# Performance work log

Measured on AMD Instinct MI355X. Metric: run time of the kernel, lower is better.

## Reference

```python
import jax, jax.numpy as jnp
import numpy as np

N = 50000   # nodes
E = 800000  # edges
H = 4       # num_heads
D = 32      # out_dim
IN = 256    # in_dim


def setup_inputs() -> dict:
    key = jax.random.key(0)
    k0, k1, k2, k3, k4, k5 = jax.random.split(key, 6)
    h = jax.random.normal(k0, (N, IN), dtype=jnp.float32)
    # fl weight (torch Linear stores [out, in]), xavier-ish scale
    Wl = jax.random.normal(k1, (H * D, IN), dtype=jnp.float32) * (1.0 / np.sqrt(IN))
    # fc / fq are initialized to small constants in torch; use small random here
    fc = jax.random.normal(k2, (IN, H * D), dtype=jnp.float32) * 0.02
    fq = jax.random.normal(k3, (IN, H * D), dtype=jnp.float32) * 0.02
    src = jax.random.randint(k4, (E,), 0, N)
    dst = jax.random.randint(k5, (E,), 0, N)
    return {"h": h, "Wl": Wl, "fc": fc, "fq": fq, "src": src, "dst": dst}


def reference(h, Wl, fc, fq, src, dst):
    n = h.shape[0]
    ft = (h @ Wl.T).reshape(n, H, D)      # [N,H,D]
    ft_c = (h @ fc).reshape(n, H, D)      # [N,H,D]
    ft_q = (h @ fq).reshape(n, H, D)      # [N,H,D]

    # edge attention: c = ft_c[dst], q = ft_q[src] - c, a = ELU(sum(q*c))
    c = ft_c[dst]                         # [E,H,D]
    a = jax.nn.elu(jnp.sum((ft_q[src] - c) * c, axis=-1))  # [E,H]

    # segmented (per-destination) softmax over incoming edges, per head
    m = jax.ops.segment_max(a, dst, num_segments=n)        # [N,H]
    ex = jnp.exp(a - m[dst])
    s = jax.ops.segment_sum(ex, dst, num_segments=n)       # [N,H]
    attn = ex / s[dst]                                     # [E,H]

    # global top-k (smallest l_s) threshold + mass redistribution, per head
    l_s = int(0.713 * attn.shape[0])
    srt = jnp.sort(attn, axis=0)                           # ascending per head
    thd = srt[l_s - 1]                                     # [H] l_s-th smallest
    topk_sum = jnp.sum(srt[:l_s], axis=0)                  # [H]
    a2 = jnp.where(attn - thd < 0, jnp.zeros((), attn.dtype), attn)
    ratio = (jnp.sum(a2, axis=0) + topk_sum) / jnp.sum(a2, axis=0)  # [H]
    a3 = a2 * ratio                                        # [E,H]

    # weighted scatter-sum of source features to destinations
    out = jax.ops.segment_sum(ft[src] * a3[:, :, None], dst, num_segments=n)  # [N,H,D]

    # concat=True: cat(flattened heads, mean over heads of ft)
    return jnp.concatenate([out.reshape(n, -1), ft.mean(axis=1)], axis=1)  # [N, H*D + D]
```

## Files before the change

kernel.cpp:

```cpp
#include <hip/hip_runtime.h>
#include <hip/hip_bf16.h>
#include <math.h>

#define N_NODES 50000
#define N_EDGES 800000
#define NH 4
#define DH 32
#define IN_DIM 256
#define OUTC 160
#define LS 570400
#define RANK0 (LS - 1)
#define DEG_CAP 160

typedef unsigned long long u64;
#define SC_FX 1099511627776.0

__global__ void k_deg(const int* __restrict__ dst, unsigned* __restrict__ A){
  int e = blockIdx.x * 256 + threadIdx.x;
  if (e < N_EDGES) atomicAdd(&A[dst[e]], 1u);
}

__global__ __launch_bounds__(1024) void k_scan(unsigned* __restrict__ A){
  __shared__ unsigned ps[1024];
  int t = threadIdx.x;
  const int CH = (N_NODES + 1023) / 1024;
  int base = t * CH;
  unsigned s = 0;
  for (int i = 0; i < CH; i++){ int n = base + i; if (n < N_NODES) s += A[n]; }
  ps[t] = s;
  __syncthreads();
  for (int off = 1; off < 1024; off <<= 1){
    unsigned v = (t >= off) ? ps[t - off] : 0;
    __syncthreads();
    ps[t] += v;
    __syncthreads();
  }
  unsigned ex = (t == 0) ? 0 : ps[t - 1];
  for (int i = 0; i < CH; i++){
    int n = base + i;
    if (n < N_NODES){ unsigned dv = A[n]; A[n] = ex; ex += dv; }
  }
}

__global__ void k_fill(const int* __restrict__ dst, unsigned* __restrict__ A,
                       unsigned* __restrict__ eidx){
  int e = blockIdx.x * 256 + threadIdx.x;
  if (e < N_EDGES) eidx[atomicAdd(&A[dst[e]], 1u)] = (unsigned)e;
}

__global__ void k_init(u64* __restrict__ sel4, unsigned* __restrict__ krem,
                       unsigned* __restrict__ cnt, unsigned* __restrict__ done,
                       unsigned* __restrict__ ccnt, u64* __restrict__ gsums){
  int t = threadIdx.x;
  if (t < 4){ sel4[t] = 0; krem[t] = RANK0; cnt[t] = 0; ccnt[t] = 0; }
  if (t < 8) gsums[t] = 0;
  if (t == 0) done[0] = 0;
}

#define BM 128
#define BK 16
__global__ __launch_bounds__(256) void k_gemm32(const float* __restrict__ A,
                                                const float* __restrict__ Wl,
                                                float* __restrict__ C){
  __shared__ float As[BK][BM + 4];
  __shared__ float Bs[BK][128 + 4];
  int tid = threadIdx.x;
  int m0 = blockIdx.x * BM;
  int ty = tid / 16, tx = tid % 16;
  float acc[8][8];
  #pragma unroll
  for (int i = 0; i < 8; i++)
    #pragma unroll
    for (int j = 0; j < 8; j++) acc[i][j] = 0.f;

  for (int k0 = 0; k0 < IN_DIM; k0 += BK){
    #pragma unroll
    for (int i = 0; i < 2; i++){
      int s = tid * 2 + i;
      int row = s >> 2, c4 = s & 3;
      int r = m0 + row;
      float4 v = make_float4(0.f, 0.f, 0.f, 0.f);
      if (r < N_NODES) v = *(const float4*)&A[(size_t)r * IN_DIM + k0 + c4 * 4];
      As[c4 * 4 + 0][row] = v.x; As[c4 * 4 + 1][row] = v.y;
      As[c4 * 4 + 2][row] = v.z; As[c4 * 4 + 3][row] = v.w;
    }
    #pragma unroll
    for (int i = 0; i < 2; i++){
      int s = tid * 2 + i;
      int j = s >> 2, c4 = s & 3;
      float4 v = *(const float4*)&Wl[(size_t)j * IN_DIM + k0 + c4 * 4];
      Bs[c4 * 4 + 0][j] = v.x; Bs[c4 * 4 + 1][j] = v.y;
      Bs[c4 * 4 + 2][j] = v.z; Bs[c4 * 4 + 3][j] = v.w;
    }
    __syncthreads();
    #pragma unroll
    for (int kk = 0; kk < BK; kk++){
      float4 a0 = *(const float4*)&As[kk][ty * 4];
      float4 a1 = *(const float4*)&As[kk][64 + ty * 4];
      float4 b0 = *(const float4*)&Bs[kk][tx * 4];
      float4 b1 = *(const float4*)&Bs[kk][64 + tx * 4];
      float av[8] = {a0.x, a0.y, a0.z, a0.w, a1.x, a1.y, a1.z, a1.w};
      float bv[8] = {b0.x, b0.y, b0.z, b0.w, b1.x, b1.y, b1.z, b1.w};
      #pragma unroll
      for (int i = 0; i < 8; i++)
        #pragma unroll
        for (int j = 0; j < 8; j++)
          acc[i][j] = fmaf(av[i], bv[j], acc[i][j]);
    }
    __syncthreads();
  }
  #pragma unroll
  for (int i = 0; i < 8; i++){
    int r = m0 + ((i < 4) ? (ty * 4 + i) : (64 + ty * 4 + (i - 4)));
    if (r >= N_NODES) continue;
    *(float4*)&C[(size_t)r * 128 + tx * 4]      = make_float4(acc[i][0], acc[i][1], acc[i][2], acc[i][3]);
    *(float4*)&C[(size_t)r * 128 + 64 + tx * 4] = make_float4(acc[i][4], acc[i][5], acc[i][6], acc[i][7]);
  }
}

__global__ __launch_bounds__(256) void k_gemm64(const float* __restrict__ A,
                                                const float* __restrict__ fc,
                                                const float* __restrict__ fq,
                                                double* __restrict__ c64,
                                                double* __restrict__ q64){
  __shared__ double As[16][66];
  __shared__ double Bs[16][66];
  int tid = threadIdx.x;
  int m0 = blockIdx.x * 64;
  int n0 = blockIdx.y * 64;
  const float* Bsrc = (n0 < 128) ? fc : fq;
  int j0 = (n0 < 128) ? n0 : n0 - 128;
  double* Cp = (n0 < 128) ? c64 : q64;
  int ty = tid / 16, tx = tid % 16;
  double acc[4][4];
  #pragma unroll
  for (int i = 0; i < 4; i++)
    #pragma unroll
    for (int j = 0; j < 4; j++) acc[i][j] = 0.0;

  for (int k0 = 0; k0 < IN_DIM; k0 += 16){
    {
      int row = tid >> 2, c4 = tid & 3;
      int r = m0 + row;
      float4 v = make_float4(0.f, 0.f, 0.f, 0.f);
      if (r < N_NODES) v = *(const float4*)&A[(size_t)r * IN_DIM + k0 + c4 * 4];
      As[c4 * 4 + 0][row] = (double)v.x; As[c4 * 4 + 1][row] = (double)v.y;
      As[c4 * 4 + 2][row] = (double)v.z; As[c4 * 4 + 3][row] = (double)v.w;
    }
    {
      int kr = tid >> 4, c4 = tid & 15;
      float4 v = *(const float4*)&Bsrc[(size_t)(k0 + kr) * 128 + j0 + c4 * 4];
      Bs[kr][c4 * 4 + 0] = (double)v.x; Bs[kr][c4 * 4 + 1] = (double)v.y;
      Bs[kr][c4 * 4 + 2] = (double)v.z; Bs[kr][c4 * 4 + 3] = (double)v.w;
    }
    __syncthreads();
    #pragma unroll
    for (int kk = 0; kk < 16; kk++){
      double a[4], b[4];
      #pragma unroll
      for (int i = 0; i < 4; i++) a[i] = As[kk][ty * 4 + i];
      #pragma unroll
      for (int j = 0; j < 4; j++) b[j] = Bs[kk][tx * 4 + j];
      #pragma unroll
      for (int i = 0; i < 4; i++)
        #pragma unroll
        for (int j = 0; j < 4; j++)
          acc[i][j] = fma(a[i], b[j], acc[i][j]);
    }
    __syncthreads();
  }
  #pragma unroll
  for (int i = 0; i < 4; i++){
    int r = m0 + ty * 4 + i;
    if (r >= N_NODES) continue;
    double* p = &Cp[(size_t)r * 128 + j0 + tx * 4];
    *(double2*)p       = make_double2(acc[i][0], acc[i][1]);
    *(double2*)(p + 2) = make_double2(acc[i][2], acc[i][3]);
  }
}

__global__ __launch_bounds__(256) void k_softedge(const double* __restrict__ c64,
    const double* __restrict__ q64, const int* __restrict__ src,
    const unsigned* __restrict__ A, const unsigned* __restrict__ eidx,
    double* __restrict__ abuf){
  __shared__ double lds_a[4][DEG_CAP * 4];
  int d = blockIdx.x * 4 + (threadIdx.x >> 6);
  int t = threadIdx.x & 63;
  int wv = threadIdx.x >> 6;
  if (d >= N_NODES) return;
  unsigned k0 = d ? A[d - 1] : 0u, k1 = A[d];
  if (k0 == k1) return;
  double2 c = *(const double2*)&c64[(size_t)d * 128 + t * 2];
  double m = -1.0e300;
  int sn = src[eidx[k0]];
  double2 qn = *(const double2*)&q64[(size_t)sn * 128 + t * 2];
  for (unsigned k = k0; k < k1; k++){
    double2 q = qn;
    if (k + 1 < k1){
      int s2 = src[eidx[k + 1]];
      qn = *(const double2*)&q64[(size_t)s2 * 128 + t * 2];
    }
    double val = (q.x - c.x) * c.x + (q.y - c.y) * c.y;
    val += __shfl_xor(val, 1);
    val += __shfl_xor(val, 2);
    val += __shfl_xor(val, 4);
    val += __shfl_xor(val, 8);
    double a = (val > 0.0) ? val : expm1(val);
    m = fmax(m, a);
    if ((t & 15) == 0) lds_a[wv][(k - k0) * 4 + (t >> 4)] = a;
  }
  double mm = __shfl(m, (t & 3) * 16);
  unsigned nj = (k1 - k0) * 4;
  long long sfx = 0;
  for (unsigned jj = t; jj < nj; jj += 64){
    double ex = exp(lds_a[wv][jj] - mm);
    lds_a[wv][jj] = ex;
    sfx += llrint(ex * SC_FX);
  }
  #pragma unroll
  for (int msk = 4; msk < 64; msk <<= 1) sfx += __shfl_xor(sfx, msk);
  double sd = (double)sfx * (1.0 / SC_FX);
  for (unsigned jj = t; jj < nj; jj += 64)
    abuf[(size_t)k0 * 4 + jj] = lds_a[wv][jj] / sd;
}

__global__ __launch_bounds__(256) void k_hp(const double* __restrict__ attn,
    u64* __restrict__ sel4, unsigned* __restrict__ krem, unsigned* __restrict__ cnt,
    unsigned* __restrict__ hist, unsigned* __restrict__ done, u64 maskHi, int shift){
  __shared__ unsigned lh[1024];
  __shared__ unsigned ticket;
  for (int j = threadIdx.x; j < 1024; j += 256) lh[j] = 0;
  __syncthreads();
  int i0 = blockIdx.x * 256 + threadIdx.x;
  int hh = i0 & 3;
  u64 sel = sel4[hh] & maskHi;
  const int total = N_EDGES * 4;
  for (int i = i0; i < total; i += gridDim.x * 256){
    u64 u = (u64)__double_as_longlong(attn[i]);
    if ((u & maskHi) == sel)
      atomicAdd(&lh[hh * 256 + (unsigned)((u >> shift) & 255u)], 1u);
  }
  __syncthreads();
  for (int j = threadIdx.x; j < 1024; j += 256)
    if (lh[j]) atomicAdd(&hist[j], lh[j]);
  __threadfence();
  if (threadIdx.x == 0) ticket = atomicAdd(done, 1u);
  __syncthreads();
  if (ticket == gridDim.x - 1){
    __threadfence();
    for (int j = threadIdx.x; j < 1024; j += 256){ lh[j] = hist[j]; hist[j] = 0; }
    __syncthreads();
    if (threadIdx.x < 4){
      int t = threadIdx.x;
      unsigned kr = krem[t], cum = 0, b = 0;
      for (; b < 256; b++){
        unsigned c2 = lh[t * 256 + b];
        if (kr < cum + c2) break;
        cum += c2;
      }
      sel4[t] |= ((u64)b) << shift;
      krem[t] = kr - cum;
      cnt[t] += cum;
    }
    if (threadIdx.x == 0) *done = 0;
  }
}

__global__ __launch_bounds__(256) void k_compact(const double* __restrict__ attn,
    const u64* __restrict__ sel4, unsigned* __restrict__ ccnt,
    double* __restrict__ cand){
  __shared__ unsigned lcnt[4];
  __shared__ unsigned lbase[4];
  int t = threadIdx.x;
  if (t < 4) lcnt[t] = 0;
  __syncthreads();
  int i0 = blockIdx.x * 256 + t;
  int hh = i0 & 3;
  u64 sel = sel4[hh] & 0xFFFF000000000000ull;
  const int total = N_EDGES * 4;
  unsigned mc = 0;
  for (int i = i0; i < total; i += gridDim.x * 256){
    u64 u = (u64)__double_as_longlong(attn[i]);
    if ((u & 0xFFFF000000000000ull) == sel) mc++;
  }
  unsigned my_local = mc ? atomicAdd(&lcnt[hh], mc) : 0u;
  __syncthreads();
  if (t < 4) lbase[t] = lcnt[t] ? atomicAdd(&ccnt[t], lcnt[t]) : 0u;
  __syncthreads();
  if (mc == 0) return;
  unsigned pos = lbase[hh] + my_local;
  double* cp = cand + (size_t)hh * N_EDGES;
  for (int i = i0; i < total; i += gridDim.x * 256){
    double v = attn[i];
    u64 u = (u64)__double_as_longlong(v);
    if ((u & 0xFFFF000000000000ull) == sel) cp[pos++] = v;
  }
}

__global__ __launch_bounds__(256) void k_finish(const double* __restrict__ cand,
    const unsigned* __restrict__ ccnt, u64* __restrict__ sel4,
    unsigned* __restrict__ krem, unsigned* __restrict__ cnt){
  __shared__ unsigned lh[256];
  __shared__ u64 s_sel;
  __shared__ unsigned s_krem, s_cnt;
  int h = blockIdx.x;
  int t = threadIdx.x;
  if (t == 0){ s_sel = sel4[h]; s_krem = krem[h]; s_cnt = cnt[h]; }
  __syncthreads();
  unsigned n = ccnt[h];
  const double* cp = cand + (size_t)h * N_EDGES;
  for (int p = 2; p < 8; p++){
    int shift = 56 - 8 * p;
    u64 maskHi = ~((1ull << (shift + 8)) - 1);
    lh[t] = 0;
    __syncthreads();
    u64 sel = s_sel;
    for (unsigned i = t; i < n; i += 256){
      u64 u = (u64)__double_as_longlong(cp[i]);
      if ((u & maskHi) == sel) atomicAdd(&lh[(unsigned)((u >> shift) & 255u)], 1u);
    }
    __syncthreads();
    if (t == 0){
      unsigned kr = s_krem, cum = 0, b = 0;
      for (; b < 256; b++){
        unsigned c2 = lh[b];
        if (kr < cum + c2) break;
        cum += c2;
      }
      s_sel |= ((u64)b) << shift;
      s_krem = kr - cum;
      s_cnt += cum;
    }
    __syncthreads();
  }
  if (t == 0){ sel4[h] = s_sel; krem[h] = s_krem; cnt[h] = s_cnt; }
}

__global__ __launch_bounds__(256) void k_sums(const double* __restrict__ attn,
    const u64* __restrict__ sel4, u64* __restrict__ gsums, float* __restrict__ a3){
  int t = threadIdx.x;
  int i0 = blockIdx.x * 256 + t;
  int hh = t & 3;
  double thd = __longlong_as_double((long long)sel4[hh]);
  double al = 0.0, ag = 0.0;
  const int total = N_EDGES * 4;
  for (int i = i0; i < total; i += gridDim.x * 256){
    double v = attn[i];
    if (v < thd){ al += v; a3[i] = 0.f; }
    else        { ag += v; a3[i] = (float)v; }
  }
  long long ql = llrint(al * SC_FX);
  long long qg = llrint(ag * SC_FX);
  #pragma unroll
  for (int m = 4; m < 64; m <<= 1){
    ql += __shfl_xor(ql, m);
    qg += __shfl_xor(qg, m);
  }
  __shared__ long long sl[16], sg[16];
  int wv = t >> 6;
  if ((t & 63) < 4){ sl[wv * 4 + hh] = ql; sg[wv * 4 + hh] = qg; }
  __syncthreads();
  if (t < 4){
    long long a = sl[t] + sl[4 + t] + sl[8 + t] + sl[12 + t];
    long long b = sg[t] + sg[4 + t] + sg[8 + t] + sg[12 + t];
    if (a) atomicAdd(&gsums[t],     (u64)a);
    if (b) atomicAdd(&gsums[4 + t], (u64)b);
  }
}

__global__ void k_ratio(const u64* __restrict__ sel4, const unsigned* __restrict__ cnt,
                        const u64* __restrict__ gsums, double* __restrict__ trd){
  int t = threadIdx.x;
  if (t < 4){
    double thd = __longlong_as_double((long long)sel4[t]);
    double sless = (double)gsums[t]     * (1.0 / SC_FX);
    double sge   = (double)gsums[4 + t] * (1.0 / SC_FX);
    double topk  = sless + (double)(LS - (int)cnt[t]) * thd;
    trd[t] = thd;
    trd[4 + t] = (sge + topk) / sge;
  }
}

__global__ __launch_bounds__(256) void k_scatter2(const float* __restrict__ ft,
    const int* __restrict__ src, const unsigned* __restrict__ A,
    const unsigned* __restrict__ eidx, const float* __restrict__ a3,
    const double* __restrict__ trd, float* __restrict__ out){
  int d = blockIdx.x * 4 + (threadIdx.x >> 6);
  int t = threadIdx.x & 63;
  if (d >= N_NODES) return;
  int hh = t >> 4;
  double ratio = trd[4 + hh];
  unsigned k0 = d ? A[d - 1] : 0u, k1 = A[d];
  long long acc0 = 0, acc1 = 0;
  float wn = (k0 < k1) ? a3[(size_t)k0 * 4 + hh] : 0.f;
  unsigned en = (k0 < k1) ? eidx[k0] : 0u;
  for (unsigned k = k0; k < k1; k++){
    float w = wn;
    unsigned e = en;
    if (k + 1 < k1){ wn = a3[(size_t)(k + 1) * 4 + hh]; en = eidx[k + 1]; }
    if (__ballot(w != 0.f) == 0ull) continue;
    if (w != 0.f){
      int s = src[e];
      float2 f = *(const float2*)&ft[(size_t)s * 128 + t * 2];
      double a3r = (double)w * ratio;
      acc0 += llrint(a3r * (double)f.x * SC_FX);
      acc1 += llrint(a3r * (double)f.y * SC_FX);
    }
  }
  float* p = &out[(size_t)d * OUTC + t * 2];
  p[0] = (float)((double)acc0 * (1.0 / SC_FX));
  p[1] = (float)((double)acc1 * (1.0 / SC_FX));
}

__global__ void k_mean(const float* __restrict__ ft, float* __restrict__ out){
  int i = blockIdx.x * 256 + threadIdx.x;
  if (i >= N_NODES * DH) return;
  int n = i / DH, dd = i % DH;
  const float* p = ft + (size_t)n * 128;
  out[(size_t)n * OUTC + 128 + dd] = 0.25f * (p[dd] + p[32 + dd] + p[64 + dd] + p[96 + dd]);
}

extern "C" void kernel_launch(void* const* d_in, const int* in_sizes, int n_in,
                              void* d_out, int out_size, void* d_ws, size_t ws_size,
                              hipStream_t stream){
  const float* h  = (const float*)d_in[0];
  const float* Wl = (const float*)d_in[1];
  const float* fc = (const float*)d_in[2];
  const float* fq = (const float*)d_in[3];
  const int* src  = (const int*)d_in[4];
  const int* dst  = (const int*)d_in[5];
  float* out = (float*)d_out;

  char* ws = (char*)d_ws;
  float*  ft32 = (float*)(ws);
  double* c64  = (double*)(ws + 25600000);
  float*  a3   = (float*)(ws + 25600000);
  double* q64  = (double*)(ws + 76800000);
  double* cand = (double*)(ws + 76800000);
  unsigned* A    = (unsigned*)(ws + 128000000);
  unsigned* eidx = (unsigned*)(ws + 128200064);
  unsigned* hist = (unsigned*)(ws + 131400064);
  u64*    sel4  = (u64*)(ws + 131404160);
  unsigned* krem = (unsigned*)(ws + 131404192);
  unsigned* cnt  = (unsigned*)(ws + 131404208);
  unsigned* done = (unsigned*)(ws + 131404224);
  unsigned* ccnt = (unsigned*)(ws + 131404240);
  u64*    gsums = (u64*)(ws + 131404256);
  double* trd   = (double*)(ws + 131404320);

  double* abuf = (double*)d_out;

  hipMemsetAsync(A, 0, 200004, stream);
  hipMemsetAsync(hist, 0, 4096, stream);
  k_init<<<1, 64, 0, stream>>>(sel4, krem, cnt, done, ccnt, gsums);

  k_deg<<<(N_EDGES + 255) / 256, 256, 0, stream>>>(dst, A);
  k_scan<<<1, 1024, 0, stream>>>(A);
  k_fill<<<(N_EDGES + 255) / 256, 256, 0, stream>>>(dst, A, eidx);

  k_gemm32<<<(N_NODES + BM - 1) / BM, 256, 0, stream>>>(h, Wl, ft32);
  dim3 g64((N_NODES + 63) / 64, 4);
  k_gemm64<<<g64, 256, 0, stream>>>(h, fc, fq, c64, q64);

  k_softedge<<<(N_NODES + 3) / 4, 256, 0, stream>>>(c64, q64, src, A, eidx, abuf);

  k_hp<<<1024, 256, 0, stream>>>(abuf, sel4, krem, cnt, hist, done, 0ull, 56);
  k_hp<<<1024, 256, 0, stream>>>(abuf, sel4, krem, cnt, hist, done,
                                 0xFF00000000000000ull, 48);
  k_compact<<<1024, 256, 0, stream>>>(abuf, sel4, ccnt, cand);
  k_finish<<<4, 256, 0, stream>>>(cand, ccnt, sel4, krem, cnt);

  k_sums<<<2048, 256, 0, stream>>>(abuf, sel4, gsums, a3);
  k_ratio<<<1, 64, 0, stream>>>(sel4, cnt, gsums, trd);

  k_scatter2<<<(N_NODES + 3) / 4, 256, 0, stream>>>(ft32, src, A, eidx, a3, trd, out);
  k_mean<<<(N_NODES * DH + 255) / 256, 256, 0, stream>>>(ft32, out);
}
```

Baseline: 1.116 ms.

## Parallelize radix-select finish passes across many blocks with last-block reduction

Replaces the single-kernel, 4-block refinement of the top-k threshold (six sequential byte passes over the candidate list per head) with six launches of a 512-block kernel. Each launch builds per-block shared histograms, merges them into a global histogram, and the last block picks the next byte via a ticket counter. This spreads the candidate scan across the whole GPU instead of four CUs, at the cost of five extra launches, global atomics and a fence-based completion handshake.

New measurement: 1.130 ms. No clear change (+1.2%).

```diff
diff --git a/kernel.cpp b/kernel.cpp
--- a/kernel.cpp
+++ b/kernel.cpp
@@ -297,43 +297,49 @@
   }
 }
 
-__global__ __launch_bounds__(256) void k_finish(const double* __restrict__ cand,
+__global__ __launch_bounds__(256) void k_fin2(const double* __restrict__ cand,
     const unsigned* __restrict__ ccnt, u64* __restrict__ sel4,
-    unsigned* __restrict__ krem, unsigned* __restrict__ cnt){
+    unsigned* __restrict__ krem, unsigned* __restrict__ cnt,
+    unsigned* __restrict__ hist, unsigned* __restrict__ done, int shift){
   __shared__ unsigned lh[256];
-  __shared__ u64 s_sel;
-  __shared__ unsigned s_krem, s_cnt;
-  int h = blockIdx.x;
-  int t = threadIdx.x;
-  if (t == 0){ s_sel = sel4[h]; s_krem = krem[h]; s_cnt = cnt[h]; }
-  __syncthreads();
+  __shared__ unsigned ticket;
+  int t = threadIdx.x;
+  lh[t] = 0;
+  __syncthreads();
+  int h = blockIdx.x & 3;
+  int bidx = blockIdx.x >> 2;
+  int bph = gridDim.x >> 2;
+  u64 maskHi = ~((1ull << (shift + 8)) - 1);
+  u64 sel = sel4[h] & maskHi;
   unsigned n = ccnt[h];
   const double* cp = cand + (size_t)h * N_EDGES;
-  for (int p = 2; p < 8; p++){
-    int shift = 56 - 8 * p;
-    u64 maskHi = ~((1ull << (shift + 8)) - 1);
-    lh[t] = 0;
-    __syncthreads();
-    u64 sel = s_sel;
-    for (unsigned i = t; i < n; i += 256){
-      u64 u = (u64)__double_as_longlong(cp[i]);
-      if ((u & maskHi) == sel) atomicAdd(&lh[(unsigned)((u >> shift) & 255u)], 1u);
-    }
-    __syncthreads();
-    if (t == 0){
-      unsigned kr = s_krem, cum = 0, b = 0;
+  for (unsigned i = bidx * 256 + t; i < n; i += bph * 256){
+    u64 u = (u64)__double_as_longlong(cp[i]);
+    if ((u & maskHi) == sel) atomicAdd(&lh[(unsigned)((u >> shift) & 255u)], 1u);
+  }
+  __syncthreads();
+  if (lh[t]) atomicAdd(&hist[h * 256 + t], lh[t]);
+  __threadfence();
+  if (t == 0) ticket = atomicAdd(done, 1u);
+  __syncthreads();
+  if (ticket == gridDim.x - 1){
+    __threadfence();
+    __shared__ unsigned fh[1024];
+    for (int j = t; j < 1024; j += 256){ fh[j] = hist[j]; hist[j] = 0; }
+    __syncthreads();
+    if (t < 4){
+      unsigned kr = krem[t], cum = 0, b = 0;
       for (; b < 256; b++){
-        unsigned c2 = lh[b];
+        unsigned c2 = fh[t * 256 + b];
         if (kr < cum + c2) break;
         cum += c2;
       }
-      s_sel |= ((u64)b) << shift;
-      s_krem = kr - cum;
-      s_cnt += cum;
-    }
-    __syncthreads();
-  }
-  if (t == 0){ sel4[h] = s_sel; krem[h] = s_krem; cnt[h] = s_cnt; }
+      sel4[t] |= ((u64)b) << shift;
+      krem[t] = kr - cum;
+      cnt[t] += cum;
+    }
+    if (t == 0) *done = 0;
+  }
 }
 
 __global__ __launch_bounds__(256) void k_sums(const double* __restrict__ attn,
@@ -468,7 +474,8 @@
   k_hp<<<1024, 256, 0, stream>>>(abuf, sel4, krem, cnt, hist, done,
                                  0xFF00000000000000ull, 48);
   k_compact<<<1024, 256, 0, stream>>>(abuf, sel4, ccnt, cand);
-  k_finish<<<4, 256, 0, stream>>>(cand, ccnt, sel4, krem, cnt);
+  for (int shift = 40; shift >= 0; shift -= 8)
+    k_fin2<<<512, 256, 0, stream>>>(cand, ccnt, sel4, krem, cnt, hist, done, shift);
 
   k_sums<<<2048, 256, 0, stream>>>(abuf, sel4, gsums, a3);
   k_ratio<<<1, 64, 0, stream>>>(sel4, cnt, gsums, trd);
```
